# Kernel tuning notes

Hardware: AMD Instinct MI355X
Metric: run time of the kernel (lower is better)

The kernel has to match this reference:

```python
import jax, jax.numpy as jnp
import numpy as np

E = 8      # num_expert
D = 1024   # d_model
H = 2048   # expert hidden (htoh4 size)
K = 2      # top_k
N = 2048   # tokens (batch*seq)


def setup_inputs() -> dict:
    key = jax.random.key(0)
    ks = jax.random.split(key, 4)
    sc = lambda k, shape, s: jax.random.normal(k, shape, jnp.float32) * s
    return {
        "inp": jax.random.normal(ks[0], (N, D), jnp.float32),
        "Wg": sc(ks[1], (D, E), D ** -0.5),          # NaiveGate linear
        "bg": jnp.zeros((E,), jnp.float32),
        "W1": sc(ks[2], (E, D, H), D ** -0.5),        # per-expert htoh4
        "b1": jnp.zeros((E, H), jnp.float32),
        "W2": sc(ks[3], (E, H, D), H ** -0.5),        # per-expert h4toh
        "b2": jnp.zeros((E, D), jnp.float32),
    }


def reference(inp, Wg, bg, W1, b1, W2, b2):
    # NaiveGate: linear -> top_k logits -> softmax over the k selected logits
    logits = inp @ Wg + bg                              # [N, E]
    top_val, top_idx = jax.lax.top_k(logits, K)         # [N, K]
    gate_score = jax.nn.softmax(top_val, axis=-1)       # [N, K]

    # Expert grouped compute. Reference computes every expert on every token
    # (exact math, no capacity dropping); combine selects the routed ones.
    h = jax.nn.gelu(jnp.einsum('nd,edh->neh', inp, W1) + b1)   # [N, E, H]
    y = jnp.einsum('neh,ehd->ned', h, W2) + b2                 # [N, E, D]

    # Combine: equivalent to bmm(gate_score[N,1,K], x[N,K,D]) after gather.
    comb = jnp.sum(jax.nn.one_hot(top_idx, E, dtype=inp.dtype)
                   * gate_score[..., None], axis=1)            # [N, E]
    return jnp.einsum('ne,ned->nd', comb, y)                   # [N, D]
```

## Files before the change

kernel.cpp:

```cpp
#include <hip/hip_runtime.h>
#include <math.h>

#define N_TOK 2048
#define DM    1024
#define HD    2048
#define NE    8
#define RMAX  5120
#define TMAX  40

#define GATE_BLKS 512
#define XCVT_BLKS 1024
#define WCVT_PER  256
#define PREP_BLKS (GATE_BLKS + XCVT_BLKS + 16 * WCVT_PER)

typedef short short8 __attribute__((ext_vector_type(8)));
typedef unsigned short u16x8 __attribute__((ext_vector_type(8)));
typedef float f32x4  __attribute__((ext_vector_type(4)));

__device__ inline unsigned short f2b(float f) {
  unsigned int u = __float_as_uint(f);
  return (unsigned short)((u + 0x7FFFu + ((u >> 16) & 1u)) >> 16);
}
__device__ inline float b2f(unsigned short s) {
  return __uint_as_float(((unsigned int)s) << 16);
}
__device__ inline void gload_lds16(const void* g, void* l) {
  __builtin_amdgcn_global_load_lds(
      (const __attribute__((address_space(1))) unsigned int*)g,
      (__attribute__((address_space(3))) unsigned int*)l, 16, 0, 0);
}

__global__ __launch_bounds__(256) void prep_kernel(
    const float* __restrict__ inp, const float* __restrict__ Wg,
    const float* __restrict__ bg,  const float* __restrict__ W1,
    const float* __restrict__ W2,
    int* __restrict__ top_idx, float* __restrict__ gate_w,
    unsigned short* __restrict__ Xb,
    unsigned short* __restrict__ W1C, unsigned short* __restrict__ W2C) {
  int bid = blockIdx.x;
  if (bid < GATE_BLKS) {
    int wave = threadIdx.x >> 6;
    int lane = threadIdx.x & 63;
    int n = bid * 4 + wave;
    float acc[NE];
#pragma unroll
    for (int e = 0; e < NE; ++e) acc[e] = 0.f;
    const float4* wg4 = reinterpret_cast<const float4*>(Wg);
#pragma unroll
    for (int i = 0; i < DM / 64; ++i) {
      int d = i * 64 + lane;
      float x = inp[n * DM + d];
      float4 w0 = wg4[d * 2 + 0];
      float4 w1 = wg4[d * 2 + 1];
      acc[0] += x * w0.x; acc[1] += x * w0.y; acc[2] += x * w0.z; acc[3] += x * w0.w;
      acc[4] += x * w1.x; acc[5] += x * w1.y; acc[6] += x * w1.z; acc[7] += x * w1.w;
    }
#pragma unroll
    for (int off = 32; off > 0; off >>= 1) {
#pragma unroll
      for (int e = 0; e < NE; ++e) acc[e] += __shfl_xor(acc[e], off);
    }
    if (lane == 0) {
      float v0 = -1e30f, v1 = -1e30f; int i0 = -1, i1 = -1;
#pragma unroll
      for (int e = 0; e < NE; ++e) {
        float v = acc[e] + bg[e];
        if (v > v0)      { v1 = v0; i1 = i0; v0 = v; i0 = e; }
        else if (v > v1) { v1 = v;  i1 = e; }
      }
      float e1 = expf(v1 - v0);
      float s  = 1.f + e1;
      top_idx[n * 2]     = i0;
      top_idx[n * 2 + 1] = i1;
      gate_w[n * 2]      = 1.f / s;
      gate_w[n * 2 + 1]  = e1 / s;
    }
  } else if (bid < GATE_BLKS + XCVT_BLKS) {
    int i = ((bid - GATE_BLKS) * 256 + threadIdx.x) * 8;
    float4 a = *(const float4*)(inp + i);
    float4 b = *(const float4*)(inp + i + 4);
    ushort4 pa, pb;
    pa.x = f2b(a.x); pa.y = f2b(a.y); pa.z = f2b(a.z); pa.w = f2b(a.w);
    pb.x = f2b(b.x); pb.y = f2b(b.y); pb.z = f2b(b.z); pb.w = f2b(b.w);
    *(ushort4*)(Xb + i)     = pa;
    *(ushort4*)(Xb + i + 4) = pb;
  } else {
    int wb = bid - (GATE_BLKS + XCVT_BLKS);
    int z  = wb >> 8;
    int r  = wb & 255;
    const float* src; unsigned short* dst; int K, N, gx, gy;
    if (z < NE) {
      src = W1 + (size_t)z * DM * HD; dst = W1C + (size_t)z * DM * HD;
      K = DM; N = HD; gx = r & 7; gy = r >> 3;
    } else {
      src = W2 + (size_t)(z - NE) * HD * DM; dst = W2C + (size_t)(z - NE) * HD * DM;
      K = HD; N = DM; gx = r & 3; gy = r >> 2;
    }
    int n0 = gx * 256, k0 = gy * 32;
    int t  = threadIdx.x;
    int cg = t & 63, kg = t >> 6;
    const float* s = src + (size_t)(k0 + kg * 8) * N + n0 + cg * 4;
    float4 v[8];
#pragma unroll
    for (int i = 0; i < 8; ++i) v[i] = *(const float4*)(s + (size_t)i * N);
#pragma unroll
    for (int c = 0; c < 4; ++c) {
      u16x8 o;
      o[0] = f2b(v[0][c]); o[1] = f2b(v[1][c]); o[2] = f2b(v[2][c]); o[3] = f2b(v[3][c]);
      o[4] = f2b(v[4][c]); o[5] = f2b(v[5][c]); o[6] = f2b(v[6][c]); o[7] = f2b(v[7][c]);
      *(u16x8*)(dst + ((size_t)(k0 / 8 + kg) * N + n0 + cg * 4 + c) * 8) = o;
    }
  }
}

__global__ __launch_bounds__(1024) void group_kernel(
    const int* __restrict__ top_idx,
    int* __restrict__ token_of, int* __restrict__ inv_g,
    int* __restrict__ tile_expert, int* __restrict__ tile_row0,
    int* __restrict__ n_tiles) {
  __shared__ int s_wtot[16];
  int tid = threadIdx.x, lane = tid & 63, wid = tid >> 6;
  int base = 0, tiles = 0;
  for (int e = 0; e < NE; ++e) {
    int cnt = 0;
#pragma unroll
    for (int c0 = 0; c0 < N_TOK; c0 += 1024) {
      int n = c0 + tid;
      int t0 = top_idx[n * 2], t1 = top_idx[n * 2 + 1];
      bool f = (t0 == e) || (t1 == e);
      int k = (t0 == e) ? 0 : 1;
      unsigned long long m = __ballot(f);
      int lp = __popcll(m & ((1ull << lane) - 1ull));
      if (lane == 0) s_wtot[wid] = __popcll(m);
      __syncthreads();
      int wbase = 0, tot = 0;
#pragma unroll
      for (int w = 0; w < 16; ++w) {
        int c = s_wtot[w];
        if (w < wid) wbase += c;
        tot += c;
      }
      if (f) {
        int pos = base + cnt + wbase + lp;
        token_of[pos] = n;
        inv_g[n * 2 + k] = pos;
      }
      cnt += tot;
      __syncthreads();
    }
    int padded = (cnt + 127) & ~127;
    for (int i = cnt + tid; i < padded; i += 1024) token_of[base + i] = -1;
    if (tid == 0) {
      for (int t = 0; t < padded / 128; ++t) {
        tile_expert[tiles + t] = e;
        tile_row0[tiles + t]   = base + t * 128;
      }
    }
    tiles += padded / 128;
    base  += padded;
    __syncthreads();
  }
  if (tid == 0) n_tiles[0] = tiles;
}

__global__ __launch_bounds__(256) void ffn1_mfma(
    const unsigned short* __restrict__ Xb,
    const unsigned short* __restrict__ W1C,
    const float* __restrict__ b1,
    const unsigned short* __restrict__ zbuf,
    const int* __restrict__ token_of, const int* __restrict__ tile_expert,
    const int* __restrict__ tile_row0, const int* __restrict__ n_tiles,
    unsigned short* __restrict__ Hbuf) {
  if ((int)blockIdx.x >= n_tiles[0]) return;
  int e    = tile_expert[blockIdx.x];
  int row0 = tile_row0[blockIdx.x];
  int h0   = blockIdx.y * 64;
  __shared__ __align__(16) unsigned short Asl[128][32];
  __shared__ __align__(16) unsigned short Bsl[64][32];
  int tid = threadIdx.x, lane = tid & 63;
  int wid = tid >> 6, wr = wid >> 1, wc = wid & 1;
  int l15 = lane & 15, l4 = lane >> 4;
  int sw  = (l15 >> 1) & 3;

  int ar[2], asg[2];
  int tk[2];
#pragma unroll
  for (int q = 0; q < 2; ++q) {
    int idx = tid + q * 256;
    ar[q]  = idx >> 2;
    asg[q] = (idx & 3) ^ ((ar[q] >> 1) & 3);
    tk[q]  = token_of[row0 + ar[q]];
  }
  int bc  = tid >> 2;
  int bsg = (tid & 3) ^ ((bc >> 1) & 3);

  f32x4 acc[4][2] = {};
  const unsigned short* W1e = W1C + (size_t)e * DM * HD;

  for (int kc = 0; kc < DM; kc += 32) {
    __syncthreads();
#pragma unroll
    for (int q = 0; q < 2; ++q) {
      int idx = tid + q * 256;
      const unsigned short* ga = (tk[q] < 0)
          ? zbuf
          : Xb + (size_t)tk[q] * DM + kc + asg[q] * 8;
      gload_lds16(ga, (char*)&Asl[0][0] + (size_t)idx * 16);
    }
    {
      const unsigned short* gb =
          W1e + ((size_t)((kc >> 3) + bsg) * HD + h0 + bc) * 8;
      gload_lds16(gb, (char*)&Bsl[0][0] + (size_t)tid * 16);
    }
    __syncthreads();
    short8 a[4], b[2];
#pragma unroll
    for (int m = 0; m < 4; ++m) {
      int R = wr * 64 + m * 16 + l15;
      a[m] = *(const short8*)((const char*)&Asl[0][0] + R * 64 + ((l4 ^ sw) << 4));
    }
#pragma unroll
    for (int n = 0; n < 2; ++n) {
      int R = wc * 32 + n * 16 + l15;
      b[n] = *(const short8*)((const char*)&Bsl[0][0] + R * 64 + ((l4 ^ sw) << 4));
    }
#pragma unroll
    for (int m = 0; m < 4; ++m)
#pragma unroll
      for (int n = 0; n < 2; ++n)
        acc[m][n] = __builtin_amdgcn_mfma_f32_16x16x32_bf16(a[m], b[n], acc[m][n], 0, 0, 0);
  }

  float bias[2];
#pragma unroll
  for (int n = 0; n < 2; ++n) bias[n] = b1[e * HD + h0 + wc * 32 + n * 16 + l15];
#pragma unroll
  for (int m = 0; m < 4; ++m) {
#pragma unroll
    for (int n = 0; n < 2; ++n) {
      int col = h0 + wc * 32 + n * 16 + l15;
#pragma unroll
      for (int j = 0; j < 4; ++j) {
        int row = row0 + wr * 64 + m * 16 + l4 * 4 + j;
        float x = acc[m][n][j] + bias[n];
        float g = 0.5f * x * (1.f + tanhf(0.7978845608f * (x + 0.044715f * x * x * x)));
        Hbuf[(size_t)row * HD + col] = f2b(g);
      }
    }
  }
}

__global__ __launch_bounds__(256) void ffn2_mfma(
    const unsigned short* __restrict__ Hbuf,
    const unsigned short* __restrict__ W2C,
    const float* __restrict__ b2,
    const int* __restrict__ tile_expert, const int* __restrict__ tile_row0,
    const int* __restrict__ n_tiles,
    unsigned short* __restrict__ Ybuf) {
  if ((int)blockIdx.x >= n_tiles[0]) return;
  int e    = tile_expert[blockIdx.x];
  int row0 = tile_row0[blockIdx.x];
  int d0   = blockIdx.y * 64;
  __shared__ __align__(16) unsigned short Asl[128][32];
  __shared__ __align__(16) unsigned short Bsl[64][32];
  int tid = threadIdx.x, lane = tid & 63;
  int wid = tid >> 6, wr = wid >> 1, wc = wid & 1;
  int l15 = lane & 15, l4 = lane >> 4;
  int sw  = (l15 >> 1) & 3;

  int ar[2], asg[2];
#pragma unroll
  for (int q = 0; q < 2; ++q) {
    int idx = tid + q * 256;
    ar[q]  = idx >> 2;
    asg[q] = (idx & 3) ^ ((ar[q] >> 1) & 3);
  }
  int bc  = tid >> 2;
  int bsg = (tid & 3) ^ ((bc >> 1) & 3);

  f32x4 acc[4][2] = {};
  const unsigned short* W2e = W2C + (size_t)e * DM * HD;

  for (int kc = 0; kc < HD; kc += 32) {
    __syncthreads();
#pragma unroll
    for (int q = 0; q < 2; ++q) {
      int idx = tid + q * 256;
      const unsigned short* ga =
          Hbuf + (size_t)(row0 + ar[q]) * HD + kc + asg[q] * 8;
      gload_lds16(ga, (char*)&Asl[0][0] + (size_t)idx * 16);
    }
    {
      const unsigned short* gb =
          W2e + ((size_t)((kc >> 3) + bsg) * DM + d0 + bc) * 8;
      gload_lds16(gb, (char*)&Bsl[0][0] + (size_t)tid * 16);
    }
    __syncthreads();
    short8 a[4], b[2];
#pragma unroll
    for (int m = 0; m < 4; ++m) {
      int R = wr * 64 + m * 16 + l15;
      a[m] = *(const short8*)((const char*)&Asl[0][0] + R * 64 + ((l4 ^ sw) << 4));
    }
#pragma unroll
    for (int n = 0; n < 2; ++n) {
      int R = wc * 32 + n * 16 + l15;
      b[n] = *(const short8*)((const char*)&Bsl[0][0] + R * 64 + ((l4 ^ sw) << 4));
    }
#pragma unroll
    for (int m = 0; m < 4; ++m)
#pragma unroll
      for (int n = 0; n < 2; ++n)
        acc[m][n] = __builtin_amdgcn_mfma_f32_16x16x32_bf16(a[m], b[n], acc[m][n], 0, 0, 0);
  }

  float bias[2];
#pragma unroll
  for (int n = 0; n < 2; ++n) bias[n] = b2[e * DM + d0 + wc * 32 + n * 16 + l15];
#pragma unroll
  for (int m = 0; m < 4; ++m) {
#pragma unroll
    for (int n = 0; n < 2; ++n) {
      int col = d0 + wc * 32 + n * 16 + l15;
#pragma unroll
      for (int j = 0; j < 4; ++j) {
        int row = row0 + wr * 64 + m * 16 + l4 * 4 + j;
        Ybuf[(size_t)row * DM + col] = f2b(acc[m][n][j] + bias[n]);
      }
    }
  }
}

__global__ void combine_kernel(const unsigned short* __restrict__ Ybuf,
                               const int* __restrict__ inv_g,
                               const float* __restrict__ gate_w,
                               float* __restrict__ out) {
  int n = blockIdx.x;
  int r0 = inv_g[n * 2], r1 = inv_g[n * 2 + 1];
  float g0 = gate_w[n * 2], g1 = gate_w[n * 2 + 1];
  int i = threadIdx.x;
  ushort4 a = *(const ushort4*)(Ybuf + (size_t)r0 * DM + i * 4);
  ushort4 b = *(const ushort4*)(Ybuf + (size_t)r1 * DM + i * 4);
  float4 rv;
  rv.x = g0 * b2f(a.x) + g1 * b2f(b.x);
  rv.y = g0 * b2f(a.y) + g1 * b2f(b.y);
  rv.z = g0 * b2f(a.z) + g1 * b2f(b.z);
  rv.w = g0 * b2f(a.w) + g1 * b2f(b.w);
  *(float4*)(out + (size_t)n * DM + i * 4) = rv;
}

extern "C" void kernel_launch(void* const* d_in, const int* in_sizes, int n_in,
                              void* d_out, int out_size, void* d_ws, size_t ws_size,
                              hipStream_t stream) {
  const float* inp = (const float*)d_in[0];
  const float* Wg  = (const float*)d_in[1];
  const float* bg  = (const float*)d_in[2];
  const float* W1  = (const float*)d_in[3];
  const float* b1  = (const float*)d_in[4];
  const float* W2  = (const float*)d_in[5];
  const float* b2  = (const float*)d_in[6];
  float* out = (float*)d_out;

  char* ws = (char*)d_ws;
  size_t off = 0;
  auto alloc = [&](size_t bytes) {
    size_t o = off;
    off = (off + bytes + 255) & ~(size_t)255;
    return o;
  };
  int*   top_idx     = (int*)  (ws + alloc(N_TOK * 2 * sizeof(int)));
  float* gate_w      = (float*)(ws + alloc(N_TOK * 2 * sizeof(float)));
  int*   token_of    = (int*)  (ws + alloc(RMAX * sizeof(int)));
  int*   inv_g       = (int*)  (ws + alloc(N_TOK * 2 * sizeof(int)));
  int*   tile_expert = (int*)  (ws + alloc(TMAX * sizeof(int)));
  int*   tile_row0   = (int*)  (ws + alloc(TMAX * sizeof(int)));
  int*   n_tiles     = (int*)  (ws + alloc(sizeof(int)));
  unsigned short* zbuf = (unsigned short*)(ws + alloc(256));
  unsigned short* Xb   = (unsigned short*)(ws + alloc((size_t)N_TOK * DM * 2));
  unsigned short* W1C  = (unsigned short*)(ws + alloc((size_t)NE * DM * HD * 2));
  unsigned short* W2C  = (unsigned short*)(ws + alloc((size_t)NE * DM * HD * 2));
  unsigned short* Hbuf = (unsigned short*)(ws + alloc((size_t)RMAX * HD * 2));
  unsigned short* Ybuf = (unsigned short*)(ws + alloc((size_t)RMAX * DM * 2));
  (void)ws_size;

  hipMemsetAsync(zbuf, 0, 256, stream);
  prep_kernel<<<PREP_BLKS, 256, 0, stream>>>(inp, Wg, bg, W1, W2,
                                             top_idx, gate_w, Xb, W1C, W2C);
  group_kernel<<<1, 1024, 0, stream>>>(top_idx, token_of, inv_g,
                                       tile_expert, tile_row0, n_tiles);
  ffn1_mfma<<<dim3(TMAX, HD / 64), 256, 0, stream>>>(
      Xb, W1C, b1, zbuf, token_of, tile_expert, tile_row0, n_tiles, Hbuf);
  ffn2_mfma<<<dim3(TMAX, DM / 64), 256, 0, stream>>>(
      Hbuf, W2C, b2, tile_expert, tile_row0, n_tiles, Ybuf);
  combine_kernel<<<N_TOK, 256, 0, stream>>>(Ybuf, inv_g, gate_w, out);
}
```

Baseline: 166.4 us.

## Fuse fp32-to-bf16 weight conversion into expert GEMM tile loads

Drops the separate prep pass that converted W1 and W2 from fp32 into a packed bf16 workspace. Each FFN GEMM block now reads fp32 weight tiles straight into registers, converts them to bf16, and writes them to a new k-grouped LDS layout. This removes a full read-and-write pass over the weights, but every M-tile of an expert now re-reads fp32 weights, which doubles those bytes. The B tile also switches from async global-to-LDS loads to synchronous register loads, so more load latency is exposed inside the k-loop.

After: 168.0 us. Within noise of the previous version (+0.9%).

```diff
diff --git a/kernel.cpp b/kernel.cpp
--- a/kernel.cpp
+++ b/kernel.cpp
@@ -10,8 +10,7 @@
 
 #define GATE_BLKS 512
 #define XCVT_BLKS 1024
-#define WCVT_PER  256
-#define PREP_BLKS (GATE_BLKS + XCVT_BLKS + 16 * WCVT_PER)
+#define PREP_BLKS (GATE_BLKS + XCVT_BLKS)
 
 typedef short short8 __attribute__((ext_vector_type(8)));
 typedef unsigned short u16x8 __attribute__((ext_vector_type(8)));
@@ -32,11 +31,9 @@
 
 __global__ __launch_bounds__(256) void prep_kernel(
     const float* __restrict__ inp, const float* __restrict__ Wg,
-    const float* __restrict__ bg,  const float* __restrict__ W1,
-    const float* __restrict__ W2,
+    const float* __restrict__ bg,
     int* __restrict__ top_idx, float* __restrict__ gate_w,
-    unsigned short* __restrict__ Xb,
-    unsigned short* __restrict__ W1C, unsigned short* __restrict__ W2C) {
+    unsigned short* __restrict__ Xb) {
   int bid = blockIdx.x;
   if (bid < GATE_BLKS) {
     int wave = threadIdx.x >> 6;
@@ -75,7 +72,7 @@
       gate_w[n * 2]      = 1.f / s;
       gate_w[n * 2 + 1]  = e1 / s;
     }
-  } else if (bid < GATE_BLKS + XCVT_BLKS) {
+  } else {
     int i = ((bid - GATE_BLKS) * 256 + threadIdx.x) * 8;
     float4 a = *(const float4*)(inp + i);
     float4 b = *(const float4*)(inp + i + 4);
@@ -84,32 +81,6 @@
     pb.x = f2b(b.x); pb.y = f2b(b.y); pb.z = f2b(b.z); pb.w = f2b(b.w);
     *(ushort4*)(Xb + i)     = pa;
     *(ushort4*)(Xb + i + 4) = pb;
-  } else {
-    int wb = bid - (GATE_BLKS + XCVT_BLKS);
-    int z  = wb >> 8;
-    int r  = wb & 255;
-    const float* src; unsigned short* dst; int K, N, gx, gy;
-    if (z < NE) {
-      src = W1 + (size_t)z * DM * HD; dst = W1C + (size_t)z * DM * HD;
-      K = DM; N = HD; gx = r & 7; gy = r >> 3;
-    } else {
-      src = W2 + (size_t)(z - NE) * HD * DM; dst = W2C + (size_t)(z - NE) * HD * DM;
-      K = HD; N = DM; gx = r & 3; gy = r >> 2;
-    }
-    int n0 = gx * 256, k0 = gy * 32;
-    int t  = threadIdx.x;
-    int cg = t & 63, kg = t >> 6;
-    const float* s = src + (size_t)(k0 + kg * 8) * N + n0 + cg * 4;
-    float4 v[8];
-#pragma unroll
-    for (int i = 0; i < 8; ++i) v[i] = *(const float4*)(s + (size_t)i * N);
-#pragma unroll
-    for (int c = 0; c < 4; ++c) {
-      u16x8 o;
-      o[0] = f2b(v[0][c]); o[1] = f2b(v[1][c]); o[2] = f2b(v[2][c]); o[3] = f2b(v[3][c]);
-      o[4] = f2b(v[4][c]); o[5] = f2b(v[5][c]); o[6] = f2b(v[6][c]); o[7] = f2b(v[7][c]);
-      *(u16x8*)(dst + ((size_t)(k0 / 8 + kg) * N + n0 + cg * 4 + c) * 8) = o;
-    }
   }
 }
 
@@ -165,7 +136,7 @@
 
 __global__ __launch_bounds__(256) void ffn1_mfma(
     const unsigned short* __restrict__ Xb,
-    const unsigned short* __restrict__ W1C,
+    const float* __restrict__ W1,
     const float* __restrict__ b1,
     const unsigned short* __restrict__ zbuf,
     const int* __restrict__ token_of, const int* __restrict__ tile_expert,
@@ -176,14 +147,13 @@
   int row0 = tile_row0[blockIdx.x];
   int h0   = blockIdx.y * 64;
   __shared__ __align__(16) unsigned short Asl[128][32];
-  __shared__ __align__(16) unsigned short Bsl[64][32];
+  __shared__ __align__(16) unsigned short Bsl[4][64][8];
   int tid = threadIdx.x, lane = tid & 63;
   int wid = tid >> 6, wr = wid >> 1, wc = wid & 1;
   int l15 = lane & 15, l4 = lane >> 4;
   int sw  = (l15 >> 1) & 3;
 
-  int ar[2], asg[2];
-  int tk[2];
+  int ar[2], asg[2], tk[2];
 #pragma unroll
   for (int q = 0; q < 2; ++q) {
     int idx = tid + q * 256;
@@ -191,14 +161,17 @@
     asg[q] = (idx & 3) ^ ((ar[q] >> 1) & 3);
     tk[q]  = token_of[row0 + ar[q]];
   }
-  int bc  = tid >> 2;
-  int bsg = (tid & 3) ^ ((bc >> 1) & 3);
+  int bcol = tid & 63, bks = tid >> 6;
+  const float* bsrc = W1 + (size_t)e * DM * HD + (size_t)(bks * 8) * HD + h0 + bcol;
 
   f32x4 acc[4][2] = {};
-  const unsigned short* W1e = W1C + (size_t)e * DM * HD;
 
   for (int kc = 0; kc < DM; kc += 32) {
     __syncthreads();
+    float bv[8];
+#pragma unroll
+    for (int i = 0; i < 8; ++i) bv[i] = bsrc[(size_t)i * HD];
+    bsrc += (size_t)32 * HD;
 #pragma unroll
     for (int q = 0; q < 2; ++q) {
       int idx = tid + q * 256;
@@ -207,11 +180,10 @@
           : Xb + (size_t)tk[q] * DM + kc + asg[q] * 8;
       gload_lds16(ga, (char*)&Asl[0][0] + (size_t)idx * 16);
     }
-    {
-      const unsigned short* gb =
-          W1e + ((size_t)((kc >> 3) + bsg) * HD + h0 + bc) * 8;
-      gload_lds16(gb, (char*)&Bsl[0][0] + (size_t)tid * 16);
-    }
+    u16x8 bo;
+#pragma unroll
+    for (int i = 0; i < 8; ++i) bo[i] = f2b(bv[i]);
+    *(u16x8*)&Bsl[bks][bcol][0] = bo;
     __syncthreads();
     short8 a[4], b[2];
 #pragma unroll
@@ -220,10 +192,8 @@
       a[m] = *(const short8*)((const char*)&Asl[0][0] + R * 64 + ((l4 ^ sw) << 4));
     }
 #pragma unroll
-    for (int n = 0; n < 2; ++n) {
-      int R = wc * 32 + n * 16 + l15;
-      b[n] = *(const short8*)((const char*)&Bsl[0][0] + R * 64 + ((l4 ^ sw) << 4));
-    }
+    for (int n = 0; n < 2; ++n)
+      b[n] = *(const short8*)&Bsl[l4][wc * 32 + n * 16 + l15][0];
 #pragma unroll
     for (int m = 0; m < 4; ++m)
 #pragma unroll
@@ -252,7 +222,7 @@
 
 __global__ __launch_bounds__(256) void ffn2_mfma(
     const unsigned short* __restrict__ Hbuf,
-    const unsigned short* __restrict__ W2C,
+    const float* __restrict__ W2,
     const float* __restrict__ b2,
     const int* __restrict__ tile_expert, const int* __restrict__ tile_row0,
     const int* __restrict__ n_tiles,
@@ -262,7 +232,7 @@
   int row0 = tile_row0[blockIdx.x];
   int d0   = blockIdx.y * 64;
   __shared__ __align__(16) unsigned short Asl[128][32];
-  __shared__ __align__(16) unsigned short Bsl[64][32];
+  __shared__ __align__(16) unsigned short Bsl[4][64][8];
   int tid = threadIdx.x, lane = tid & 63;
   int wid = tid >> 6, wr = wid >> 1, wc = wid & 1;
   int l15 = lane & 15, l4 = lane >> 4;
@@ -275,14 +245,17 @@
     ar[q]  = idx >> 2;
     asg[q] = (idx & 3) ^ ((ar[q] >> 1) & 3);
   }
-  int bc  = tid >> 2;
-  int bsg = (tid & 3) ^ ((bc >> 1) & 3);
+  int bcol = tid & 63, bks = tid >> 6;
+  const float* bsrc = W2 + (size_t)e * HD * DM + (size_t)(bks * 8) * DM + d0 + bcol;
 
   f32x4 acc[4][2] = {};
-  const unsigned short* W2e = W2C + (size_t)e * DM * HD;
 
   for (int kc = 0; kc < HD; kc += 32) {
     __syncthreads();
+    float bv[8];
+#pragma unroll
+    for (int i = 0; i < 8; ++i) bv[i] = bsrc[(size_t)i * DM];
+    bsrc += (size_t)32 * DM;
 #pragma unroll
     for (int q = 0; q < 2; ++q) {
       int idx = tid + q * 256;
@@ -290,11 +263,10 @@
           Hbuf + (size_t)(row0 + ar[q]) * HD + kc + asg[q] * 8;
       gload_lds16(ga, (char*)&Asl[0][0] + (size_t)idx * 16);
     }
-    {
-      const unsigned short* gb =
-          W2e + ((size_t)((kc >> 3) + bsg) * DM + d0 + bc) * 8;
-      gload_lds16(gb, (char*)&Bsl[0][0] + (size_t)tid * 16);
-    }
+    u16x8 bo;
+#pragma unroll
+    for (int i = 0; i < 8; ++i) bo[i] = f2b(bv[i]);
+    *(u16x8*)&Bsl[bks][bcol][0] = bo;
     __syncthreads();
     short8 a[4], b[2];
 #pragma unroll
@@ -303,10 +275,8 @@
       a[m] = *(const short8*)((const char*)&Asl[0][0] + R * 64 + ((l4 ^ sw) << 4));
     }
 #pragma unroll
-    for (int n = 0; n < 2; ++n) {
-      int R = wc * 32 + n * 16 + l15;
-      b[n] = *(const short8*)((const char*)&Bsl[0][0] + R * 64 + ((l4 ^ sw) << 4));
-    }
+    for (int n = 0; n < 2; ++n)
+      b[n] = *(const short8*)&Bsl[l4][wc * 32 + n * 16 + l15][0];
 #pragma unroll
     for (int m = 0; m < 4; ++m)
 #pragma unroll
@@ -377,20 +347,17 @@
   int*   n_tiles     = (int*)  (ws + alloc(sizeof(int)));
   unsigned short* zbuf = (unsigned short*)(ws + alloc(256));
   unsigned short* Xb   = (unsigned short*)(ws + alloc((size_t)N_TOK * DM * 2));
-  unsigned short* W1C  = (unsigned short*)(ws + alloc((size_t)NE * DM * HD * 2));
-  unsigned short* W2C  = (unsigned short*)(ws + alloc((size_t)NE * DM * HD * 2));
   unsigned short* Hbuf = (unsigned short*)(ws + alloc((size_t)RMAX * HD * 2));
   unsigned short* Ybuf = (unsigned short*)(ws + alloc((size_t)RMAX * DM * 2));
   (void)ws_size;
 
   hipMemsetAsync(zbuf, 0, 256, stream);
-  prep_kernel<<<PREP_BLKS, 256, 0, stream>>>(inp, Wg, bg, W1, W2,
-                                             top_idx, gate_w, Xb, W1C, W2C);
+  prep_kernel<<<PREP_BLKS, 256, 0, stream>>>(inp, Wg, bg, top_idx, gate_w, Xb);
   group_kernel<<<1, 1024, 0, stream>>>(top_idx, token_of, inv_g,
                                        tile_expert, tile_row0, n_tiles);
   ffn1_mfma<<<dim3(TMAX, HD / 64), 256, 0, stream>>>(
-      Xb, W1C, b1, zbuf, token_of, tile_expert, tile_row0, n_tiles, Hbuf);
+      Xb, W1, b1, zbuf, token_of, tile_expert, tile_row0, n_tiles, Hbuf);
   ffn2_mfma<<<dim3(TMAX, DM / 64), 256, 0, stream>>>(
-      Hbuf, W2C, b2, tile_expert, tile_row0, n_tiles, Ybuf);
+      Hbuf, W2, b2, tile_expert, tile_row0, n_tiles, Ybuf);
   combine_kernel<<<N_TOK, 256, 0, stream>>>(Ybuf, inv_g, gate_w, out);
 }
```
